# Performance work log

Measured on AMD Instinct MI355X. Metric: run time of the kernel, lower is better.

Reference implementation:

```python
import jax, jax.numpy as jnp
import numpy as np

DIM = 33


def setup_inputs() -> dict:
    key = jax.random.key(0)
    k1, k2 = jax.random.split(key)
    # LUT param: (3, dim, dim, dim). Module inits to ones; use uniform values
    # so the reference exercises non-trivial gathers.
    lut = jax.random.uniform(k1, (3, DIM, DIM, DIM), dtype=jnp.float32)
    # Input image batch (B, C=3, W, H), values in [0, 1).
    x = jax.random.uniform(k2, (8, 3, 1920, 1080), dtype=jnp.float32)
    return {"lut": lut, "x": x}


def reference(lut, x):
    # Faithful JAX port of the trilinear.forward CUDA kernel used by Lut3D.
    dim = lut.shape[-1]
    binsize = 1.000001 / (dim - 1)
    xb = x / binsize  # (B, 3, W, H)
    idx = jnp.clip(jnp.floor(xb).astype(jnp.int32), 0, dim - 2)
    frac = xb - idx.astype(x.dtype)
    # channel 0 = r, 1 = g, 2 = b; flat id = r + g*dim + b*dim^2 -> LUT[c, b, g, r]
    rid, gid, bid = idx[:, 0], idx[:, 1], idx[:, 2]  # each (B, W, H)
    rd, gd, bd = frac[:, 0], frac[:, 1], frac[:, 2]

    def corner(db, dg, dr):
        # gather 8 neighboring LUT cells -> (3, B, W, H)
        return lut[:, bid + db, gid + dg, rid + dr]

    w000 = (1 - rd) * (1 - gd) * (1 - bd)
    w100 = rd * (1 - gd) * (1 - bd)
    w010 = (1 - rd) * gd * (1 - bd)
    w110 = rd * gd * (1 - bd)
    w001 = (1 - rd) * (1 - gd) * bd
    w101 = rd * (1 - gd) * bd
    w011 = (1 - rd) * gd * bd
    w111 = rd * gd * bd

    out = (corner(0, 0, 0) * w000 + corner(0, 0, 1) * w100
           + corner(0, 1, 0) * w010 + corner(0, 1, 1) * w110
           + corner(1, 0, 0) * w001 + corner(1, 0, 1) * w101
           + corner(1, 1, 0) * w011 + corner(1, 1, 1) * w111)  # (3, B, W, H)
    return jnp.transpose(out, (1, 0, 2, 3))  # (B, 3, W, H)
```

## Files before the change

### kernel.cpp

```cpp
#include <hip/hip_runtime.h>
#include <stdint.h>

#define DIM 33
#define D2 (DIM * DIM)
#define NENT (DIM * DIM * DIM)
#define HW 2073600
#define NIMG 8
#define HW4 (HW / 4)
#define QP (NIMG * HW4)
#define BLK 1024
#define NBLK 256
#define STRIDE (BLK * NBLK)

typedef float f32x4 __attribute__((ext_vector_type(4)));

__device__ __forceinline__ float lerpf(float a, float b, float t) {
    return fmaf(t, b - a, a);
}

__global__ __launch_bounds__(256) void build_packed10(const float* __restrict__ lut,
                                                      uint32_t* __restrict__ T) {
    int e = blockIdx.x * 256 + threadIdx.x;
    if (e >= NENT) return;
    uint32_t q0 = (uint32_t)(lut[e] * 1023.f + 0.5f);
    uint32_t q1 = (uint32_t)(lut[NENT + e] * 1023.f + 0.5f);
    uint32_t q2 = (uint32_t)(lut[2 * NENT + e] * 1023.f + 0.5f);
    T[e] = q0 | (q1 << 10) | (q2 << 20);
}

#define U0(v) ((float)((v) & 1023u))
#define U1(v) ((float)(((v) >> 10) & 1023u))
#define U2(v) ((float)((v) >> 20))

__global__ __launch_bounds__(1024) void lut3d_lds(const float* __restrict__ x,
                                                  const uint32_t* __restrict__ T,
                                                  float* __restrict__ out) {
    __shared__ uint32_t L[NENT];
    for (int e = threadIdx.x; e < NENT; e += BLK) L[e] = T[e];
    __syncthreads();

    const float inv = 32.0f / 1.000001f;
    const float qs = 1.0f / 1023.0f;

    int j = blockIdx.x * BLK + threadIdx.x;
    f32x4 R, G, B;
    {
        int img = j / HW4;
        int i = (j - img * HW4) * 4;
        const float* xp = x + (size_t)img * 3 * HW + i;
        R = *(const f32x4*)xp;
        G = *(const f32x4*)(xp + HW);
        B = *(const f32x4*)(xp + 2 * HW);
    }

    while (j < QP) {
        int jn = j + STRIDE;
        f32x4 Rn, Gn, Bn;
        if (jn < QP) {
            int img = jn / HW4;
            int i = (jn - img * HW4) * 4;
            const float* xp = x + (size_t)img * 3 * HW + i;
            Rn = *(const f32x4*)xp;
            Gn = *(const f32x4*)(xp + HW);
            Bn = *(const f32x4*)(xp + 2 * HW);
        }

        float o0[4], o1[4], o2[4];
#pragma unroll
        for (int k = 0; k < 4; ++k) {
            float xr = R[k] * inv;
            float xg = G[k] * inv;
            float xb = B[k] * inv;
            int ri = (int)xr; ri = ri > DIM - 2 ? DIM - 2 : ri;
            int gi = (int)xg; gi = gi > DIM - 2 ? DIM - 2 : gi;
            int bi = (int)xb; bi = bi > DIM - 2 ? DIM - 2 : bi;
            float rd = xr - (float)ri;
            float gd = xg - (float)gi;
            float bd = xb - (float)bi;
            int base = (bi * DIM + gi) * DIM + ri;
            uint32_t v000 = L[base],            v001 = L[base + 1];
            uint32_t v010 = L[base + DIM],      v011 = L[base + DIM + 1];
            uint32_t v100 = L[base + D2],       v101 = L[base + D2 + 1];
            uint32_t v110 = L[base + D2 + DIM], v111 = L[base + D2 + DIM + 1];

            {
                float q00 = lerpf(U0(v000), U0(v001), rd);
                float q01 = lerpf(U0(v010), U0(v011), rd);
                float q10 = lerpf(U0(v100), U0(v101), rd);
                float q11 = lerpf(U0(v110), U0(v111), rd);
                o0[k] = lerpf(lerpf(q00, q01, gd), lerpf(q10, q11, gd), bd) * qs;
            }
            {
                float q00 = lerpf(U1(v000), U1(v001), rd);
                float q01 = lerpf(U1(v010), U1(v011), rd);
                float q10 = lerpf(U1(v100), U1(v101), rd);
                float q11 = lerpf(U1(v110), U1(v111), rd);
                o1[k] = lerpf(lerpf(q00, q01, gd), lerpf(q10, q11, gd), bd) * qs;
            }
            {
                float q00 = lerpf(U2(v000), U2(v001), rd);
                float q01 = lerpf(U2(v010), U2(v011), rd);
                float q10 = lerpf(U2(v100), U2(v101), rd);
                float q11 = lerpf(U2(v110), U2(v111), rd);
                o2[k] = lerpf(lerpf(q00, q01, gd), lerpf(q10, q11, gd), bd) * qs;
            }
        }

        {
            int img = j / HW4;
            int i = (j - img * HW4) * 4;
            float* op = out + (size_t)img * 3 * HW + i;
            f32x4 v0 = {o0[0], o0[1], o0[2], o0[3]};
            f32x4 v1 = {o1[0], o1[1], o1[2], o1[3]};
            f32x4 v2 = {o2[0], o2[1], o2[2], o2[3]};
            __builtin_nontemporal_store(v0, (f32x4*)op);
            __builtin_nontemporal_store(v1, (f32x4*)(op + HW));
            __builtin_nontemporal_store(v2, (f32x4*)(op + 2 * HW));
        }

        R = Rn; G = Gn; B = Bn;
        j = jn;
    }
}

__global__ __launch_bounds__(256) void lut3d_direct(const float* __restrict__ x,
                                                    const float* __restrict__ lut,
                                                    float* __restrict__ out) {
    const int img = blockIdx.y;
    const int i = (blockIdx.x * 256 + threadIdx.x) * 4;
    const float* xp = x + (size_t)img * 3 * HW + i;
    f32x4 Rv = *(const f32x4*)xp;
    f32x4 Gv = *(const f32x4*)(xp + HW);
    f32x4 Bv = *(const f32x4*)(xp + 2 * HW);
    float o0[4], o1[4], o2[4];
    const float inv = 32.0f / 1.000001f;
#pragma unroll
    for (int k = 0; k < 4; ++k) {
        float xr = Rv[k] * inv;
        float xg = Gv[k] * inv;
        float xb = Bv[k] * inv;
        int ri = (int)xr; ri = ri < 0 ? 0 : (ri > DIM - 2 ? DIM - 2 : ri);
        int gi = (int)xg; gi = gi < 0 ? 0 : (gi > DIM - 2 ? DIM - 2 : gi);
        int bi = (int)xb; bi = bi < 0 ? 0 : (bi > DIM - 2 ? DIM - 2 : bi);
        float rd = xr - (float)ri;
        float gd = xg - (float)gi;
        float bd = xb - (float)bi;
        int base = (bi * DIM + gi) * DIM + ri;
        float oc[3];
#pragma unroll
        for (int c = 0; c < 3; ++c) {
            const float* Lp = lut + c * NENT + base;
            float v000 = Lp[0],        v001 = Lp[1];
            float v010 = Lp[DIM],      v011 = Lp[DIM + 1];
            float v100 = Lp[D2],       v101 = Lp[D2 + 1];
            float v110 = Lp[D2 + DIM], v111 = Lp[D2 + DIM + 1];
            float q0 = lerpf(v000, v001, rd);
            float q1 = lerpf(v010, v011, rd);
            float q2 = lerpf(v100, v101, rd);
            float q3 = lerpf(v110, v111, rd);
            float p0 = lerpf(q0, q1, gd);
            float p1 = lerpf(q2, q3, gd);
            oc[c] = lerpf(p0, p1, bd);
        }
        o0[k] = oc[0]; o1[k] = oc[1]; o2[k] = oc[2];
    }
    float* op = out + (size_t)img * 3 * HW + i;
    f32x4 v0 = {o0[0], o0[1], o0[2], o0[3]};
    f32x4 v1 = {o1[0], o1[1], o1[2], o1[3]};
    f32x4 v2 = {o2[0], o2[1], o2[2], o2[3]};
    *(f32x4*)op = v0;
    *(f32x4*)(op + HW) = v1;
    *(f32x4*)(op + 2 * HW) = v2;
}

extern "C" void kernel_launch(void* const* d_in, const int* in_sizes, int n_in,
                              void* d_out, int out_size, void* d_ws, size_t ws_size,
                              hipStream_t stream) {
    const float* lut = (const float*)d_in[0];
    const float* x   = (const float*)d_in[1];
    float* out = (float*)d_out;

    if (ws_size >= (size_t)NENT * 4) {
        uint32_t* T = (uint32_t*)d_ws;
        build_packed10<<<(NENT + 255) / 256, 256, 0, stream>>>(lut, T);
        lut3d_lds<<<NBLK, BLK, 0, stream>>>(x, T, out);
    } else {
        const dim3 grid(HW / 4 / 256, NIMG);
        lut3d_direct<<<grid, dim3(256), 0, stream>>>(x, lut, out);
    }
}
```

Baseline: 334.2 us.

## Process two quads per iteration with hoisted LDS gathers and overlapped prefetch

The persistent LDS kernel now handles two pixel quads per loop iteration over a fixed 8-iteration schedule. It issues all 64 LDS gathers before the next global loads and the interpolation math, to raise memory-level parallelism. The LUT copy into LDS now uses 16-byte vector loads, and the first input loads are issued before the barrier so they overlap the LUT fill. The cost is higher register pressure at 1024 threads per block, which may force spills. The fixed trip count also assumes the problem size exactly.

```diff
diff --git a/kernel.cpp b/kernel.cpp
--- a/kernel.cpp
+++ b/kernel.cpp
@@ -11,8 +11,10 @@
 #define BLK 1024
 #define NBLK 256
 #define STRIDE (BLK * NBLK)
+#define STRIDE2 (2 * STRIDE)
 
 typedef float f32x4 __attribute__((ext_vector_type(4)));
+typedef uint32_t u32x4 __attribute__((ext_vector_type(4)));
 
 __device__ __forceinline__ float lerpf(float a, float b, float t) {
     return fmaf(t, b - a, a);
@@ -32,94 +34,141 @@
 #define U1(v) ((float)(((v) >> 10) & 1023u))
 #define U2(v) ((float)((v) >> 20))
 
-__global__ __launch_bounds__(1024) void lut3d_lds(const float* __restrict__ x,
-                                                  const uint32_t* __restrict__ T,
-                                                  float* __restrict__ out) {
-    __shared__ uint32_t L[NENT];
-    for (int e = threadIdx.x; e < NENT; e += BLK) L[e] = T[e];
-    __syncthreads();
-
-    const float inv = 32.0f / 1.000001f;
-    const float qs = 1.0f / 1023.0f;
-
-    int j = blockIdx.x * BLK + threadIdx.x;
-    f32x4 R, G, B;
-    {
+__device__ __forceinline__ void loadq(const float* __restrict__ x, int j, bool valid,
+                                      f32x4& R, f32x4& G, f32x4& B) {
+    if (valid) {
         int img = j / HW4;
         int i = (j - img * HW4) * 4;
         const float* xp = x + (size_t)img * 3 * HW + i;
         R = *(const f32x4*)xp;
         G = *(const f32x4*)(xp + HW);
         B = *(const f32x4*)(xp + 2 * HW);
-    }
-
-    while (j < QP) {
-        int jn = j + STRIDE;
-        f32x4 Rn, Gn, Bn;
-        if (jn < QP) {
-            int img = jn / HW4;
-            int i = (jn - img * HW4) * 4;
-            const float* xp = x + (size_t)img * 3 * HW + i;
-            Rn = *(const f32x4*)xp;
-            Gn = *(const f32x4*)(xp + HW);
-            Bn = *(const f32x4*)(xp + 2 * HW);
-        }
-
-        float o0[4], o1[4], o2[4];
-#pragma unroll
-        for (int k = 0; k < 4; ++k) {
-            float xr = R[k] * inv;
-            float xg = G[k] * inv;
-            float xb = B[k] * inv;
-            int ri = (int)xr; ri = ri > DIM - 2 ? DIM - 2 : ri;
-            int gi = (int)xg; gi = gi > DIM - 2 ? DIM - 2 : gi;
-            int bi = (int)xb; bi = bi > DIM - 2 ? DIM - 2 : bi;
-            float rd = xr - (float)ri;
-            float gd = xg - (float)gi;
-            float bd = xb - (float)bi;
-            int base = (bi * DIM + gi) * DIM + ri;
-            uint32_t v000 = L[base],            v001 = L[base + 1];
-            uint32_t v010 = L[base + DIM],      v011 = L[base + DIM + 1];
-            uint32_t v100 = L[base + D2],       v101 = L[base + D2 + 1];
-            uint32_t v110 = L[base + D2 + DIM], v111 = L[base + D2 + DIM + 1];
-
-            {
-                float q00 = lerpf(U0(v000), U0(v001), rd);
-                float q01 = lerpf(U0(v010), U0(v011), rd);
-                float q10 = lerpf(U0(v100), U0(v101), rd);
-                float q11 = lerpf(U0(v110), U0(v111), rd);
-                o0[k] = lerpf(lerpf(q00, q01, gd), lerpf(q10, q11, gd), bd) * qs;
-            }
-            {
-                float q00 = lerpf(U1(v000), U1(v001), rd);
-                float q01 = lerpf(U1(v010), U1(v011), rd);
-                float q10 = lerpf(U1(v100), U1(v101), rd);
-                float q11 = lerpf(U1(v110), U1(v111), rd);
-                o1[k] = lerpf(lerpf(q00, q01, gd), lerpf(q10, q11, gd), bd) * qs;
-            }
-            {
-                float q00 = lerpf(U2(v000), U2(v001), rd);
-                float q01 = lerpf(U2(v010), U2(v011), rd);
-                float q10 = lerpf(U2(v100), U2(v101), rd);
-                float q11 = lerpf(U2(v110), U2(v111), rd);
-                o2[k] = lerpf(lerpf(q00, q01, gd), lerpf(q10, q11, gd), bd) * qs;
-            }
-        }
+    } else {
+        R = f32x4{0.f, 0.f, 0.f, 0.f};
+        G = f32x4{0.f, 0.f, 0.f, 0.f};
+        B = f32x4{0.f, 0.f, 0.f, 0.f};
+    }
+}
+
+__device__ __forceinline__ void idxfrac(float r, float g, float b,
+                                        int& base, float& rd, float& gd, float& bd) {
+    const float inv = 32.0f / 1.000001f;
+    float xr = r * inv;
+    float xg = g * inv;
+    float xb = b * inv;
+    int ri = (int)xr; ri = ri > DIM - 2 ? DIM - 2 : ri;
+    int gi = (int)xg; gi = gi > DIM - 2 ? DIM - 2 : gi;
+    int bi = (int)xb; bi = bi > DIM - 2 ? DIM - 2 : bi;
+    rd = xr - (float)ri;
+    gd = xg - (float)gi;
+    bd = xb - (float)bi;
+    base = (bi * DIM + gi) * DIM + ri;
+}
+
+__device__ __forceinline__ void interp(const uint32_t (&v)[8], float rd, float gd, float bd,
+                                       float& o0, float& o1, float& o2) {
+    const float qs = 1.0f / 1023.0f;
+    {
+        float q00 = lerpf(U0(v[0]), U0(v[1]), rd);
+        float q01 = lerpf(U0(v[2]), U0(v[3]), rd);
+        float q10 = lerpf(U0(v[4]), U0(v[5]), rd);
+        float q11 = lerpf(U0(v[6]), U0(v[7]), rd);
+        o0 = lerpf(lerpf(q00, q01, gd), lerpf(q10, q11, gd), bd) * qs;
+    }
+    {
+        float q00 = lerpf(U1(v[0]), U1(v[1]), rd);
+        float q01 = lerpf(U1(v[2]), U1(v[3]), rd);
+        float q10 = lerpf(U1(v[4]), U1(v[5]), rd);
+        float q11 = lerpf(U1(v[6]), U1(v[7]), rd);
+        o1 = lerpf(lerpf(q00, q01, gd), lerpf(q10, q11, gd), bd) * qs;
+    }
+    {
+        float q00 = lerpf(U2(v[0]), U2(v[1]), rd);
+        float q01 = lerpf(U2(v[2]), U2(v[3]), rd);
+        float q10 = lerpf(U2(v[4]), U2(v[5]), rd);
+        float q11 = lerpf(U2(v[6]), U2(v[7]), rd);
+        o2 = lerpf(lerpf(q00, q01, gd), lerpf(q10, q11, gd), bd) * qs;
+    }
+}
+
+__global__ __launch_bounds__(1024) void lut3d_lds(const float* __restrict__ x,
+                                                  const uint32_t* __restrict__ T,
+                                                  float* __restrict__ out) {
+    __shared__ __align__(16) uint32_t L[NENT];
+
+    {
+        const u32x4* T4 = (const u32x4*)T;
+        u32x4* L4 = (u32x4*)L;
+        for (int e = threadIdx.x; e < NENT / 4; e += BLK) L4[e] = T4[e];
+        if (threadIdx.x == 0) L[NENT - 1] = T[NENT - 1];
+    }
+
+    const int j0 = blockIdx.x * BLK + threadIdx.x;
+
+    f32x4 RA, GA, BA, RB, GB, BB;
+    loadq(x, j0, true, RA, GA, BA);
+    loadq(x, j0 + STRIDE, true, RB, GB, BB);
+
+    __syncthreads();
+
+#pragma unroll 1
+    for (int p = 0; p < 8; ++p) {
+        const int jA = j0 + p * STRIDE2;
+        const int jB = jA + STRIDE;
+        const bool vB = (jB < QP);
+
+        int base[8];
+        float rd[8], gd[8], bd[8];
+#pragma unroll
+        for (int k = 0; k < 4; ++k)
+            idxfrac(RA[k], GA[k], BA[k], base[k], rd[k], gd[k], bd[k]);
+#pragma unroll
+        for (int k = 0; k < 4; ++k)
+            idxfrac(RB[k], GB[k], BB[k], base[4 + k], rd[4 + k], gd[4 + k], bd[4 + k]);
+
+        uint32_t v[8][8];
+#pragma unroll
+        for (int k = 0; k < 8; ++k) {
+            const int b0 = base[k];
+            v[k][0] = L[b0];            v[k][1] = L[b0 + 1];
+            v[k][2] = L[b0 + DIM];      v[k][3] = L[b0 + DIM + 1];
+            v[k][4] = L[b0 + D2];       v[k][5] = L[b0 + D2 + 1];
+            v[k][6] = L[b0 + D2 + DIM]; v[k][7] = L[b0 + D2 + DIM + 1];
+        }
+
+        if (p < 7) {
+            const int jA2 = jA + STRIDE2;
+            loadq(x, jA2, true, RA, GA, BA);
+            loadq(x, jA2 + STRIDE, jA2 + STRIDE < QP, RB, GB, BB);
+        }
+
+        float o[8][3];
+#pragma unroll
+        for (int k = 0; k < 8; ++k)
+            interp(v[k], rd[k], gd[k], bd[k], o[k][0], o[k][1], o[k][2]);
 
         {
-            int img = j / HW4;
-            int i = (j - img * HW4) * 4;
+            const int img = jA / HW4;
+            const int i = (jA - img * HW4) * 4;
             float* op = out + (size_t)img * 3 * HW + i;
-            f32x4 v0 = {o0[0], o0[1], o0[2], o0[3]};
-            f32x4 v1 = {o1[0], o1[1], o1[2], o1[3]};
-            f32x4 v2 = {o2[0], o2[1], o2[2], o2[3]};
+            f32x4 v0 = {o[0][0], o[1][0], o[2][0], o[3][0]};
+            f32x4 v1 = {o[0][1], o[1][1], o[2][1], o[3][1]};
+            f32x4 v2 = {o[0][2], o[1][2], o[2][2], o[3][2]};
             __builtin_nontemporal_store(v0, (f32x4*)op);
             __builtin_nontemporal_store(v1, (f32x4*)(op + HW));
             __builtin_nontemporal_store(v2, (f32x4*)(op + 2 * HW));
         }
-
-        R = Rn; G = Gn; B = Bn;
-        j = jn;
+        if (vB) {
+            const int img = jB / HW4;
+            const int i = (jB - img * HW4) * 4;
+            float* op = out + (size_t)img * 3 * HW + i;
+            f32x4 v0 = {o[4][0], o[5][0], o[6][0], o[7][0]};
+            f32x4 v1 = {o[4][1], o[5][1], o[6][1], o[7][1]};
+            f32x4 v2 = {o[4][2], o[5][2], o[6][2], o[7][2]};
+            __builtin_nontemporal_store(v0, (f32x4*)op);
+            __builtin_nontemporal_store(v1, (f32x4*)(op + HW));
+            __builtin_nontemporal_store(v2, (f32x4*)(op + 2 * HW));
+        }
     }
 }
 
```

After: 376.2 us. 12.6% more time.
